# Kernel optimization log

Hardware: AMD Instinct MI355X
Metric: run time of the kernel (lower is better)

The kernel has to match this reference:

```python
import jax, jax.numpy as jnp
import numpy as np
import math

FACTOR = 3.0

def setup_inputs() -> dict:
    key = jax.random.key(0)
    k1, k2, k3 = jax.random.split(key, 3)
    B, L, H, E = 16, 4096, 8, 64
    queries = jax.random.normal(k1, (B, L, H, E), dtype=jnp.float32)
    keys = jax.random.normal(k2, (B, L, H, E), dtype=jnp.float32)
    values = jax.random.normal(k3, (B, L, H, E), dtype=jnp.float32)
    return {"queries": queries, "keys": keys, "values": values}

def reference(queries, keys, values):
    B, L, H, E = queries.shape
    top_k = int(FACTOR * math.log(L))  # 24 for L=4096 (static)
    # [B,H,E,L] layout for FFT along time
    q = jnp.transpose(queries, (0, 2, 3, 1))
    k = jnp.transpose(keys, (0, 2, 3, 1))
    v = jnp.transpose(values, (0, 2, 3, 1))
    # period-based autocorrelation via FFT cross-correlation
    qf = jnp.fft.rfft(q, axis=-1)
    kf = jnp.fft.rfft(k, axis=-1)
    corr = jnp.fft.irfft(qf * jnp.conj(kf), n=L, axis=-1)  # [B,H,E,L]
    # training-mode aggregation: shared top-k delay indices across batch
    mean_value = corr.mean(axis=(1, 2))                # [B,L]
    _, index = jax.lax.top_k(mean_value.mean(axis=0), top_k)  # [top_k]
    weights = mean_value[:, index]                     # [B,top_k]
    tmp_corr = jax.nn.softmax(weights, axis=-1)        # [B,top_k]
    delays_agg = jnp.zeros_like(v)
    for i in range(top_k):  # small static loop over delays
        pattern = jnp.roll(v, -index[i], axis=-1)
        delays_agg = delays_agg + pattern * tmp_corr[:, i][:, None, None, None]
    V = jnp.transpose(delays_agg, (0, 3, 1, 2))        # [B,L,H,E]
    return V
```

## Files before the change

kernel.cpp:

```cpp
#include <hip/hip_runtime.h>
#include <math.h>

#define B_ 16
#define L_ 4096
#define H_ 8
#define E_ 64
#define C_ 512
#define K_ 24
#define NT 256
#define RPAD 257
#define PSTRIDE 2052
#define G_ 64

__device__ __forceinline__ float2 cmul(float2 a, float2 b) {
    return make_float2(a.x * b.x - a.y * b.y, a.x * b.y + a.y * b.x);
}
__device__ __forceinline__ float2 cadd(float2 a, float2 b) { return make_float2(a.x + b.x, a.y + b.y); }
__device__ __forceinline__ float2 csub(float2 a, float2 b) { return make_float2(a.x - b.x, a.y - b.y); }

__device__ __forceinline__ void bar_lds() {
    asm volatile("s_waitcnt lgkmcnt(0)" ::: "memory");
    __builtin_amdgcn_s_barrier();
}

__device__ __forceinline__ void fft16(float2 a[16]) {
    const float r2 = 0.70710678118654752f;
    const float c1 = 0.92387953251128676f;
    const float s1 = 0.38268343236508977f;
    const float2 W16[8] = {
        make_float2(1.f, 0.f),  make_float2(c1, -s1),  make_float2(r2, -r2),  make_float2(s1, -c1),
        make_float2(0.f, -1.f), make_float2(-s1, -c1), make_float2(-r2, -r2), make_float2(-c1, -s1)};
    #pragma unroll
    for (int j = 0; j < 8; ++j) {
        float2 u = a[j], v = a[j + 8];
        a[j]     = cadd(u, v);
        a[j + 8] = cmul(csub(u, v), W16[j]);
    }
    #pragma unroll
    for (int b = 0; b < 16; b += 8)
        #pragma unroll
        for (int j = 0; j < 4; ++j) {
            float2 u = a[b + j], v = a[b + j + 4];
            a[b + j]     = cadd(u, v);
            a[b + j + 4] = cmul(csub(u, v), W16[2 * j]);
        }
    #pragma unroll
    for (int b = 0; b < 16; b += 4)
        #pragma unroll
        for (int j = 0; j < 2; ++j) {
            float2 u = a[b + j], v = a[b + j + 2];
            a[b + j]     = cadd(u, v);
            a[b + j + 2] = cmul(csub(u, v), W16[4 * j]);
        }
    #pragma unroll
    for (int b = 0; b < 16; b += 2) {
        float2 u = a[b], v = a[b + 1];
        a[b]     = cadd(u, v);
        a[b + 1] = csub(u, v);
    }
}

__global__ __launch_bounds__(256) void k_phaseA(const float* __restrict__ q,
                                                const float* __restrict__ k,
                                                float2* __restrict__ z,
                                                int b0) {
    __shared__ float2 s2[256 * 17];
    const int br4[16] = {0, 8, 4, 12, 2, 10, 6, 14, 1, 9, 5, 13, 3, 11, 7, 15};
    int w  = blockIdx.x;
    int g  = blockIdx.y;
    int bl = blockIdx.z;
    int b  = b0 + bl;
    int tid = threadIdx.x;

    const size_t base = (size_t)b * L_ * C_ + g * 16;
    int lrow = tid >> 2;
    int lq   = tid & 3;
    #pragma unroll
    for (int it = 0; it < 4; ++it) {
        int r   = lrow + (it << 6);
        int tau = ((r >> 4) << 8) + (w << 4) + (r & 15);
        const float4 q4 = *(const float4*)(q + base + (size_t)tau * C_ + (lq << 2));
        const float4 k4 = *(const float4*)(k + base + (size_t)tau * C_ + (lq << 2));
        float2* dst = &s2[r * 17 + (lq << 2)];
        dst[0] = make_float2(q4.x, k4.x);
        dst[1] = make_float2(q4.y, k4.y);
        dst[2] = make_float2(q4.z, k4.z);
        dst[3] = make_float2(q4.w, k4.w);
    }
    __syncthreads();

    int ch = tid >> 4, n2loc = tid & 15;
    int n2 = (w << 4) + n2loc;
    float2 a[16];
    int rbase = n2loc * 17 + ch;
    #pragma unroll
    for (int n1 = 0; n1 < 16; ++n1) a[n1] = s2[n1 * 272 + rbase];
    fft16(a);
    float sn, cs;
    sincospif((float)n2 / 2048.0f, &sn, &cs);
    const float2 w1 = make_float2(cs, -sn);
    const float2 w2 = cmul(w1, w1);
    const float2 w4 = cmul(w2, w2);
    float2 tws[4] = {w1, w2, cmul(w2, w1), w4};
    float2* zc = z + ((size_t)bl * C_ + (g * 16 + ch)) * L_ + n2;
    zc[0] = a[0];
    #pragma unroll
    for (int k1 = 1; k1 < 16; ++k1) {
        int j = (k1 - 1) & 3;
        zc[(size_t)(k1 << 8)] = cmul(a[br4[k1]], tws[j]);
        tws[j] = cmul(tws[j], w4);
    }
}

__global__ __launch_bounds__(256) void k_fft_bc(const float2* __restrict__ z,
                                                float2* __restrict__ part,
                                                int b0) {
    __shared__ float2 s[16 * RPAD];
    __shared__ float2 tw256[256];
    const int br4[16] = {0, 8, 4, 12, 2, 10, 6, 14, 1, 9, 5, 13, 3, 11, 7, 15};
    int t  = threadIdx.x;
    int bl = blockIdx.y;
    int b  = b0 + bl;
    int g  = blockIdx.x;
    int c0 = g * 8;

    {
        int r1 = t >> 4, m2 = t & 15;
        float sn, cs;
        sincospif((float)(r1 * m2) / 128.0f, &sn, &cs);
        tw256[t] = make_float2(cs, -sn);
    }
    float accx[8], accy[8], accN = 0.f;
    #pragma unroll
    for (int r = 0; r < 8; ++r) { accx[r] = 0.f; accy[r] = 0.f; }

    const int rowB = t >> 4, m2B = t & 15;
    const int k1C = t & 15, r1C = t >> 4;

    float2 a[16];
    {
        const float2* zc0 = z + ((size_t)bl * C_ + c0) * L_;
        #pragma unroll
        for (int m1 = 0; m1 < 16; ++m1) a[m1] = zc0[(rowB << 8) + (m1 << 4) + m2B];
    }
    bar_lds();

    for (int cc = 0; cc < 8; ++cc) {
        fft16(a);
        #pragma unroll
        for (int r1 = 0; r1 < 16; ++r1)
            s[rowB * RPAD + (r1 << 4) + m2B] = cmul(a[br4[r1]], tw256[(r1 << 4) + m2B]);
        __syncthreads();
        #pragma unroll
        for (int m2 = 0; m2 < 16; ++m2) a[m2] = s[k1C * RPAD + (r1C << 4) + m2];
        fft16(a);
        __syncthreads();
        #pragma unroll
        for (int r2 = 0; r2 < 16; ++r2)
            s[(r2 << 8) + (r1C << 4) + k1C] = a[br4[r2]];
        if (cc < 7) {
            const float2* zn = z + ((size_t)bl * C_ + (c0 + cc + 1)) * L_;
            #pragma unroll
            for (int m1 = 0; m1 < 16; ++m1) a[m1] = zn[(rowB << 8) + (m1 << 4) + m2B];
        }
        bar_lds();
        #pragma unroll
        for (int r = 0; r < 8; ++r) {
            int p  = t + (r << 8);
            int pp = (L_ - p) & (L_ - 1);
            float2 A  = s[p];
            float2 Bv = s[pp];
            float Qr = 0.5f * (A.x + Bv.x);
            float Qi = 0.5f * (A.y - Bv.y);
            float Kr = 0.5f * (A.y + Bv.y);
            float Ki = 0.5f * (A.x - Bv.x);
            accx[r] += Qr * Kr - Qi * Ki;
            accy[r] += Qr * Ki + Qi * Kr;
        }
        accN += s[2048].x * s[2048].y;
        bar_lds();
    }
    float2* pb = part + (size_t)(b * G_ + g) * PSTRIDE;
    #pragma unroll
    for (int r = 0; r < 8; ++r)
        pb[t + (r << 8)] = make_float2(accx[r], accy[r]);
    if (t == 0) pb[2048] = make_float2(accN, 0.f);
}

__global__ __launch_bounds__(256) void k_reduce(const float2* __restrict__ part,
                                                float* __restrict__ cross) {
    __shared__ float2 acc2[128];
    int b  = blockIdx.x;
    int pt = blockIdx.y;
    int t  = threadIdx.x;
    int pi = t & 127, gh = t >> 7;
    int p  = pt * 128 + pi;
    float sx = 0.f, sy = 0.f;
    if (p <= 2048) {
        const float2* base = part + ((size_t)b * G_ + gh * 32) * PSTRIDE + p;
        #pragma unroll 4
        for (int g = 0; g < 32; ++g) {
            float2 v = base[(size_t)g * PSTRIDE];
            sx += v.x; sy += v.y;
        }
    }
    if (gh == 1) acc2[pi] = make_float2(sx, sy);
    __syncthreads();
    if (gh == 0 && p <= 2048) {
        float2 o = acc2[pi];
        ((float2*)cross)[(size_t)b * L_ + p] = make_float2(sx + o.x, sy + o.y);
    }
}

__global__ __launch_bounds__(256) void k_ifft(const float* __restrict__ cross,
                                              float* __restrict__ mv) {
    __shared__ float2 s[16 * RPAD];
    __shared__ float2 tw256[256];
    const int br4[16] = {0, 8, 4, 12, 2, 10, 6, 14, 1, 9, 5, 13, 3, 11, 7, 15};
    int t = threadIdx.x;
    int b = blockIdx.x;
    {
        int r1 = t >> 4, m2 = t & 15;
        float sn, cs;
        sincospif((float)(r1 * m2) / 128.0f, &sn, &cs);
        tw256[t] = make_float2(cs, -sn);
    }
    const float2* cr = (const float2*)cross + (size_t)b * L_;
    float2 a[16];
    #pragma unroll
    for (int n1 = 0; n1 < 16; ++n1) {
        int P = (n1 << 8) + t;
        int hi = P > 2048;
        float2 v = cr[hi ? (L_ - P) : P];
        a[n1] = hi ? v : make_float2(v.x, -v.y);
    }
    fft16(a);
    {
        float sn, cs;
        sincospif((float)t / 2048.0f, &sn, &cs);
        const float2 w1 = make_float2(cs, -sn);
        float2 tw = w1;
        s[t] = a[0];
        #pragma unroll
        for (int k1 = 1; k1 < 16; ++k1) {
            s[k1 * RPAD + t] = cmul(a[br4[k1]], tw);
            tw = cmul(tw, w1);
        }
    }
    __syncthreads();
    const int rowB = t >> 4, m2B = t & 15;
    #pragma unroll
    for (int m1 = 0; m1 < 16; ++m1) a[m1] = s[rowB * RPAD + (m1 << 4) + m2B];
    fft16(a);
    #pragma unroll
    for (int r1 = 0; r1 < 16; ++r1)
        s[rowB * RPAD + (r1 << 4) + m2B] = cmul(a[br4[r1]], tw256[(r1 << 4) + m2B]);
    __syncthreads();
    const int k1C = t & 15, r1C = t >> 4;
    #pragma unroll
    for (int m2 = 0; m2 < 16; ++m2) a[m2] = s[k1C * RPAD + (r1C << 4) + m2];
    fft16(a);
    const float scale = 1.0f / ((float)L_ * (float)C_);
    #pragma unroll
    for (int r2 = 0; r2 < 16; ++r2)
        mv[(size_t)b * L_ + (r2 << 8) + t] = a[br4[r2]].x * scale;
}

__global__ __launch_bounds__(256) void k_topk(const float* __restrict__ mv,
                                              int* __restrict__ idx,
                                              float* __restrict__ wts) {
    __shared__ float wv[4];
    __shared__ int   wi[4];
    __shared__ int   idxL[K_];
    int tid = threadIdx.x;
    float vloc[16];
    #pragma unroll
    for (int r = 0; r < 16; ++r) {
        int tt = tid + (r << 8);
        float ssum = 0.f;
        for (int b = 0; b < B_; ++b) ssum += mv[(size_t)b * L_ + tt];
        vloc[r] = ssum;
    }
    int lane = tid & 63, w = tid >> 6;
    for (int i = 0; i < K_; ++i) {
        float best = -INFINITY; int bi = 1 << 30;
        #pragma unroll
        for (int r = 0; r < 16; ++r) {
            float v = vloc[r]; int ii = tid + (r << 8);
            if (v > best || (v == best && ii < bi)) { best = v; bi = ii; }
        }
        #pragma unroll
        for (int off = 32; off > 0; off >>= 1) {
            float ov = __shfl_down(best, off);
            int   oi = __shfl_down(bi, off);
            if (ov > best || (ov == best && oi < bi)) { best = ov; bi = oi; }
        }
        if (lane == 0) { wv[w] = best; wi[w] = bi; }
        __syncthreads();
        if (tid == 0) {
            float bb = wv[0]; int bj = wi[0];
            for (int j = 1; j < 4; ++j)
                if (wv[j] > bb || (wv[j] == bb && wi[j] < bj)) { bb = wv[j]; bj = wi[j]; }
            idxL[i] = bj; idx[i] = bj;
        }
        __syncthreads();
        int win = idxL[i];
        #pragma unroll
        for (int r = 0; r < 16; ++r)
            if (win == tid + (r << 8)) vloc[r] = -INFINITY;
    }
    if (tid < B_) {
        int b = tid;
        float ww[K_]; float wm = -INFINITY;
        for (int i = 0; i < K_; ++i) { ww[i] = mv[(size_t)b * L_ + idxL[i]]; wm = fmaxf(wm, ww[i]); }
        float ssum = 0.f;
        for (int i = 0; i < K_; ++i) { ww[i] = expf(ww[i] - wm); ssum += ww[i]; }
        float inv = 1.f / ssum;
        for (int i = 0; i < K_; ++i) wts[b * K_ + i] = ww[i] * inv;
    }
}

__global__ __launch_bounds__(256) void k_agg(const float* __restrict__ vals,
                                             const int* __restrict__ idx,
                                             const float* __restrict__ wts,
                                             float* __restrict__ out) {
    __shared__ float4 sv[L_];
    __shared__ int   di[K_];
    __shared__ float dw[K_];
    const int tid = threadIdx.x;
    int id = blockIdx.x;
    int wk = ((id & 7) << 8) | (id >> 3);
    int b  = wk >> 7;
    int c0 = (wk & 127) << 2;

    if (tid < K_) { di[tid] = idx[tid]; dw[tid] = wts[b * K_ + tid]; }

    const float* gbase = vals + (size_t)b * L_ * C_ + c0;
    #pragma unroll
    for (int it = 0; it < 16; ++it) {
        int tau = (it << 8) + tid;
        const float* g = gbase + (size_t)tau * C_;
        float4* l = &sv[(it << 8) + ((tid >> 6) << 6)];
        __builtin_amdgcn_global_load_lds(
            (const __attribute__((address_space(1))) uint32_t*)g,
            (__attribute__((address_space(3))) uint32_t*)l,
            16, 0, 0);
    }
    __syncthreads();

    int   dir[K_]; float dwr[K_];
    #pragma unroll
    for (int i = 0; i < K_; ++i) { dir[i] = di[i]; dwr[i] = dw[i]; }

    float* obase = out + (size_t)b * L_ * C_ + c0;
    for (int r = 0; r < 16; ++r) {
        int tau = (r << 8) + tid;
        float4 acc = make_float4(0.f, 0.f, 0.f, 0.f);
        #pragma unroll
        for (int i = 0; i < K_; ++i) {
            float4 x = sv[(tau + dir[i]) & (L_ - 1)];
            float w = dwr[i];
            acc.x = fmaf(w, x.x, acc.x);
            acc.y = fmaf(w, x.y, acc.y);
            acc.z = fmaf(w, x.z, acc.z);
            acc.w = fmaf(w, x.w, acc.w);
        }
        *(float4*)(obase + (size_t)tau * C_) = acc;
    }
}

extern "C" void kernel_launch(void* const* d_in, const int* in_sizes, int n_in,
                              void* d_out, int out_size, void* d_ws, size_t ws_size,
                              hipStream_t stream) {
    const float* q = (const float*)d_in[0];
    const float* k = (const float*)d_in[1];
    const float* v = (const float*)d_in[2];
    float* out = (float*)d_out;
    char* ws = (char*)d_ws;

    float*  cross = (float*)ws;
    float*  mv    = (float*)(ws + (1 << 20));
    int*    idx   = (int*)(ws + (1 << 20) + (1 << 18));
    float*  wts   = (float*)(ws + (1 << 20) + (1 << 18) + 4096);
    float2* part  = (float2*)(ws + (2 << 20));
    float2* z     = (float2*)(ws + (size_t)(20 << 20));

    size_t zcap = (ws_size > (size_t)(20 << 20)) ? ws_size - (size_t)(20 << 20) : 0;
    int P = 16;
    while (P > 1 && (size_t)P * C_ * L_ * sizeof(float2) > zcap) P >>= 1;

    for (int b0 = 0; b0 < B_; b0 += P) {
        dim3 g1(16, 32, P);
        k_phaseA<<<g1, 256, 0, stream>>>(q, k, z, b0);
        dim3 g2(G_, P);
        k_fft_bc<<<g2, 256, 0, stream>>>(z, part, b0);
    }
    dim3 gr(B_, 17);
    k_reduce<<<gr, 256, 0, stream>>>(part, cross);
    k_ifft<<<B_, 256, 0, stream>>>(cross, mv);
    k_topk<<<1, 256, 0, stream>>>(mv, idx, wts);
    k_agg<<<B_ * (C_ / 4), 256, 0, stream>>>(v, idx, wts, out);
}
```

Measured before the change: 329.2 us.

## Double-buffer phase-A loads via direct global-to-LDS copies with swizzled layout

The first FFT stage kernel now processes four column blocks per workgroup, double-buffering q and k tiles in LDS with global_load_lds asynchronous copies so the next tile's load overlaps the current FFT. The LDS layout is XOR-swizzled instead of padded to avoid bank conflicts, and block IDs are remapped across XCDs. This cuts the grid size by four and adds more LDS per block (64KB), which may reduce occupancy.

```diff
diff --git a/kernel.cpp b/kernel.cpp
--- a/kernel.cpp
+++ b/kernel.cpp
@@ -64,52 +64,86 @@
                                                 const float* __restrict__ k,
                                                 float2* __restrict__ z,
                                                 int b0) {
-    __shared__ float2 s2[256 * 17];
+    __shared__ float qbuf[2][4096];
+    __shared__ float kbuf[2][4096];
     const int br4[16] = {0, 8, 4, 12, 2, 10, 6, 14, 1, 9, 5, 13, 3, 11, 7, 15};
-    int w  = blockIdx.x;
-    int g  = blockIdx.y;
-    int bl = blockIdx.z;
-    int b  = b0 + bl;
-    int tid = threadIdx.x;
-
-    const size_t base = (size_t)b * L_ * C_ + g * 16;
-    int lrow = tid >> 2;
-    int lq   = tid & 3;
-    #pragma unroll
-    for (int it = 0; it < 4; ++it) {
-        int r   = lrow + (it << 6);
-        int tau = ((r >> 4) << 8) + (w << 4) + (r & 15);
-        const float4 q4 = *(const float4*)(q + base + (size_t)tau * C_ + (lq << 2));
-        const float4 k4 = *(const float4*)(k + base + (size_t)tau * C_ + (lq << 2));
-        float2* dst = &s2[r * 17 + (lq << 2)];
-        dst[0] = make_float2(q4.x, k4.x);
-        dst[1] = make_float2(q4.y, k4.y);
-        dst[2] = make_float2(q4.z, k4.z);
-        dst[3] = make_float2(q4.w, k4.w);
-    }
-    __syncthreads();
-
-    int ch = tid >> 4, n2loc = tid & 15;
-    int n2 = (w << 4) + n2loc;
-    float2 a[16];
-    int rbase = n2loc * 17 + ch;
-    #pragma unroll
-    for (int n1 = 0; n1 < 16; ++n1) a[n1] = s2[n1 * 272 + rbase];
-    fft16(a);
-    float sn, cs;
-    sincospif((float)n2 / 2048.0f, &sn, &cs);
-    const float2 w1 = make_float2(cs, -sn);
-    const float2 w2 = cmul(w1, w1);
-    const float2 w4 = cmul(w2, w2);
-    float2 tws[4] = {w1, w2, cmul(w2, w1), w4};
-    float2* zc = z + ((size_t)bl * C_ + (g * 16 + ch)) * L_ + n2;
-    zc[0] = a[0];
-    #pragma unroll
-    for (int k1 = 1; k1 < 16; ++k1) {
-        int j = (k1 - 1) & 3;
-        zc[(size_t)(k1 << 8)] = cmul(a[br4[k1]], tws[j]);
-        tws[j] = cmul(tws[j], w4);
-    }
+    const int tid = threadIdx.x;
+
+    int id  = blockIdx.x;
+    int nb8 = gridDim.x >> 3;
+    int wk  = (id & 7) * nb8 + (id >> 3);
+    int bl  = wk >> 7;
+    int wb  = (wk >> 5) & 3;
+    int g   = wk & 31;
+    int b   = b0 + bl;
+
+    const size_t cbase = (size_t)b * L_ * C_ + g * 16;
+
+    const int srow  = tid >> 2;
+    const int squad = tid & 3;
+    const int sn2l  = srow & 15;
+    const int sqd   = squad ^ (sn2l & 3);
+    const int ldoff = ((tid >> 6) << 8);
+
+    const int ch = tid >> 4, n2loc = tid & 15;
+    const int col = (((ch >> 2) ^ (n2loc & 3)) << 2) + (ch & 3);
+    const int tb  = (n2loc << 4) + col;
+
+    #define STAGE(dbuf, w)                                                          \
+        {                                                                            \
+            const float* qw = q + cbase + (size_t)((w) << 4) * C_;                   \
+            const float* kw = k + cbase + (size_t)((w) << 4) * C_;                   \
+            _Pragma("unroll")                                                        \
+            for (int it = 0; it < 4; ++it) {                                         \
+                int r  = (it << 6) + srow;                                           \
+                size_t gof = (size_t)(((r >> 4) << 8) + (r & 15)) * C_ + (sqd << 2); \
+                float* ql = &qbuf[dbuf][(it << 10) + ldoff];                         \
+                float* kl = &kbuf[dbuf][(it << 10) + ldoff];                         \
+                __builtin_amdgcn_global_load_lds(                                    \
+                    (const __attribute__((address_space(1))) uint32_t*)(qw + gof),   \
+                    (__attribute__((address_space(3))) uint32_t*)ql, 16, 0, 0);      \
+                __builtin_amdgcn_global_load_lds(                                    \
+                    (const __attribute__((address_space(1))) uint32_t*)(kw + gof),   \
+                    (__attribute__((address_space(3))) uint32_t*)kl, 16, 0, 0);      \
+            }                                                                        \
+        }
+
+    STAGE(0, (wb << 2));
+
+    #pragma unroll
+    for (int wi = 0; wi < 4; ++wi) {
+        const int cur = wi & 1;
+        const int w   = (wb << 2) + wi;
+        if (wi < 3) STAGE(cur ^ 1, w + 1);
+        if (wi < 3) asm volatile("s_waitcnt vmcnt(8)" ::: "memory");
+        else        asm volatile("s_waitcnt vmcnt(0)" ::: "memory");
+        __builtin_amdgcn_s_barrier();
+
+        float2 a[16];
+        #pragma unroll
+        for (int n1 = 0; n1 < 16; ++n1) {
+            int ix = (n1 << 8) + tb;
+            a[n1] = make_float2(qbuf[cur][ix], kbuf[cur][ix]);
+        }
+        fft16(a);
+        int n2 = (w << 4) + n2loc;
+        float sn, cs;
+        sincospif((float)n2 / 2048.0f, &sn, &cs);
+        const float2 w1 = make_float2(cs, -sn);
+        const float2 w2 = cmul(w1, w1);
+        const float2 w4 = cmul(w2, w2);
+        float2 tws[4] = {w1, w2, cmul(w2, w1), w4};
+        float2* zc = z + ((size_t)bl * C_ + (g * 16 + ch)) * L_ + n2;
+        zc[0] = a[0];
+        #pragma unroll
+        for (int k1 = 1; k1 < 16; ++k1) {
+            int j = (k1 - 1) & 3;
+            zc[(size_t)(k1 << 8)] = cmul(a[br4[k1]], tws[j]);
+            tws[j] = cmul(tws[j], w4);
+        }
+        bar_lds();
+    }
+    #undef STAGE
 }
 
 __global__ __launch_bounds__(256) void k_fft_bc(const float2* __restrict__ z,
@@ -390,8 +424,7 @@
     while (P > 1 && (size_t)P * C_ * L_ * sizeof(float2) > zcap) P >>= 1;
 
     for (int b0 = 0; b0 < B_; b0 += P) {
-        dim3 g1(16, 32, P);
-        k_phaseA<<<g1, 256, 0, stream>>>(q, k, z, b0);
+        k_phaseA<<<128 * P, 256, 0, stream>>>(q, k, z, b0);
         dim3 g2(G_, P);
         k_fft_bc<<<g2, 256, 0, stream>>>(z, part, b0);
     }
```

Measured after the change: 331.9 us. No clear change (+0.8%).
